# Optimization experiments

Hardware: AMD Instinct MI355X
Metric: run time of the kernel (lower is better)

The kernel has to match this reference:

```python
import jax, jax.numpy as jnp
import numpy as np

N = 50000      # nodes
E = 800000     # edges per relation
R = 3          # relations
FEAT = 64      # feat_len
HID = 64       # h_dim
NUM_PRED = 5
S = 8192       # seeds


def setup_inputs() -> dict:
    key = jax.random.key(0)
    ks = jax.random.split(key, 24)
    p = lambda k, s: jax.random.normal(k, s, jnp.float32) * 0.05
    x = jax.random.normal(ks[0], (N, FEAT), jnp.float32)
    noise = jax.random.normal(ks[1], (N, HID), jnp.float32)
    seeds = jax.random.randint(ks[2], (S,), 0, N)
    edges = [jax.random.randint(ks[3 + i], (E,), 0, N) for i in range(2 * R)]
    return dict(
        x=x, noise=noise, seeds=seeds,
        src0=edges[0], dst0=edges[1], src1=edges[2], dst1=edges[3],
        src2=edges[4], dst2=edges[5],
        W_conv1=p(ks[9], (R, FEAT, HID)), b_conv1=jnp.zeros((HID,), jnp.float32),
        W_conv2=p(ks[10], (R, HID, HID)), b_conv2=jnp.zeros((HID,), jnp.float32),
        W_lin=p(ks[11], (HID, HID)), b_lin=jnp.zeros((HID,), jnp.float32),
        dW1=p(ks[12], (R, HID, 256)), db1=jnp.zeros((R, 256), jnp.float32),
        dW2=p(ks[13], (R, 256, 32)), db2=jnp.zeros((R, 32), jnp.float32),
        dW3=p(ks[14], (R, 32, 1)), db3=jnp.zeros((R, 1), jnp.float32),
        fW1=p(ks[15], (R, HID, 256)), fb1=jnp.zeros((R, 256), jnp.float32),
        fW2=p(ks[16], (R, 256, 2048)), fb2=jnp.zeros((R, 2048), jnp.float32),
        fW3=p(ks[17], (R, 2048, FEAT * NUM_PRED)), fb3=jnp.zeros((R, FEAT * NUM_PRED), jnp.float32),
    )


def _rel_conv(h, srcs, dsts, W, b):
    # DGL RelGraphConvLayer: per-relation GraphConv(norm='right'), summed over
    # relations (HeteroGraphConv aggregate='sum'), + bias, ReLU (dropout=0).
    out_dim = W.shape[2]
    acc = jnp.zeros((N, out_dim), h.dtype)
    for r in range(R):
        m = (h @ W[r])[srcs[r]]                                   # [E, out]
        agg = jnp.zeros((N, out_dim), h.dtype).at[dsts[r]].add(m)
        deg = jnp.zeros((N,), h.dtype).at[dsts[r]].add(1.0)
        acc = acc + agg / jnp.maximum(deg, 1.0)[:, None]          # norm='right'
    return jax.nn.relu(acc + b)


def reference(x, noise, W_conv1, b_conv1, W_conv2, b_conv2, W_lin, b_lin,
              dW1, db1, dW2, db2, dW3, db3,
              fW1, fb1, fW2, fb2, fW3, fb3,
              seeds, src0, dst0, src1, dst1, src2, dst2):
    srcs = (src0, src1, src2)
    dsts = (dst0, dst1, dst2)
    # two stacked relational conv layers
    h = _rel_conv(x, srcs, dsts, W_conv1, b_conv1)
    h = _rel_conv(h, srcs, dsts, W_conv2, b_conv2)
    # per-ntype Linear + LeakyReLU (dropout=0)
    h = jax.nn.leaky_relu(h @ W_lin + b_lin)
    # Sampler: additive Gaussian noise
    h = h + noise
    # dGen/fGen index inputs[ntype][ind] with ind = enumerate position -> first S rows
    hs = h[:seeds.shape[0]]                                       # [S, HID]
    # ReldGen: per-relation MLP HID->256->32->1 (LeakyReLU, final ReLU)
    z = jax.nn.leaky_relu(jnp.einsum('sd,rdh->rsh', hs, dW1) + db1[:, None, :])
    z = jax.nn.leaky_relu(jnp.einsum('rsh,rhk->rsk', z, dW2) + db2[:, None, :])
    pred_missing = jax.nn.relu(jnp.einsum('rsk,rko->rso', z, dW3) + db3[:, None, :])  # [R,S,1]
    # RelfGen: per-relation MLP HID->256->2048->FEAT*NUM_PRED (ReLU, final Tanh)
    z = jax.nn.relu(jnp.einsum('sd,rdh->rsh', hs, fW1) + fb1[:, None, :])
    z = jax.nn.relu(jnp.einsum('rsh,rhk->rsk', z, fW2) + fb2[:, None, :])
    pred_feat = jnp.tanh(jnp.einsum('rsk,rko->rso', z, fW3) + fb3[:, None, :])        # [R,S,NUM_PRED*FEAT]
    # pack (pred_missing, pred_feat) into one array [R, S, 1 + NUM_PRED*FEAT]
    return jnp.concatenate([pred_missing, pred_feat], axis=-1)
```

## Files before the change

### kernel.cpp

```cpp
#include <hip/hip_runtime.h>
#include <math.h>

#define N_NODES 50000
#define N_EDGES 800000
#define RELS    3
#define HID     64
#define S_SEEDS 8192
#define OUT_COLS 321
#define S_CH    4096
#define NB      391
#define BCAP    2560
#define CHUNK   4096
#define NCHUNK  196

typedef __attribute__((ext_vector_type(8))) _Float16 v8h;
typedef __attribute__((ext_vector_type(4))) float v4f;

__device__ __forceinline__ unsigned short f32_to_f16(float f) {
    _Float16 h = (_Float16)f;
    return __builtin_bit_cast(unsigned short, h);
}
__device__ __forceinline__ float f16_to_f32(unsigned short u) {
    return (float)__builtin_bit_cast(_Float16, u);
}

template<int ACT, bool OUT_F16, int BN, int BM = 128>
__global__ __launch_bounds__(256) void gemm_mfma_f16(
    const unsigned short* __restrict__ A, long long sAb, int lda,
    const unsigned short* __restrict__ Bt, long long sBb,
    const float* __restrict__ bias, long long sBiasb,
    void* __restrict__ Cv, long long sCb, int ldc,
    const float* __restrict__ noise,
    int M, int Nc, int K)
{
    constexpr int WC = (BN == 128 || BM == 64) ? 2 : 1;
    constexpr int WR = 4 / WC;
    constexpr int TI = BM / (WR * 16);
    constexpr int TJ = BN / (WC * 16);
    constexpr int TPRA = 256 / BM;
    constexpr int TPRB = 256 / BN;

    __shared__ __align__(16) unsigned short As[2][BM][40];
    __shared__ __align__(16) unsigned short Bs[2][BN][40];

    const int r = blockIdx.z;
    A  += (long long)r * sAb;
    Bt += (long long)r * sBb;
    const float* brow = bias ? bias + (long long)r * sBiasb : nullptr;

    const int tid  = threadIdx.x;
    const int wave = tid >> 6, lane = tid & 63;
    const int quad = lane >> 4, l16 = lane & 15;
    const int wrow = (wave / WC) * (TI * 16);
    const int wcol = (wave % WC) * (TJ * 16);
    const int row0 = blockIdx.y * BM, col0 = blockIdx.x * BN;

    v4f acc[TI][TJ] = {};

    const int srow = tid / TPRA;
    const int ecol = (tid % TPRA) * (32 / TPRA);
    const int brw  = tid / TPRB;
    const int bcl  = (tid % TPRB) * (32 / TPRB);

    const int gr = row0 + srow;
    const bool aval = (gr < M);
    const unsigned short* aptr = A + (long long)gr * lda + ecol;
    const int gn = col0 + brw;
    const bool bval = (gn < Nc);
    const unsigned short* bptr = Bt + (long long)gn * K + bcl;

    int4 a0, a1, b0, b1;
    auto loadT = [&](int k0) {
        a0 = make_int4(0, 0, 0, 0); a1 = make_int4(0, 0, 0, 0);
        b0 = make_int4(0, 0, 0, 0); b1 = make_int4(0, 0, 0, 0);
        if (aval) {
            a0 = *(const int4*)(aptr + k0);
            if constexpr (TPRA == 2) a1 = *(const int4*)(aptr + k0 + 8);
        }
        if (bval) {
            b0 = *(const int4*)(bptr + k0);
            if constexpr (TPRB == 2) b1 = *(const int4*)(bptr + k0 + 8);
        }
    };
    auto storeT = [&](int buf) {
        *(int4*)(&As[buf][srow][ecol]) = a0;
        if constexpr (TPRA == 2) *(int4*)(&As[buf][srow][ecol + 8]) = a1;
        *(int4*)(&Bs[buf][brw][bcl]) = b0;
        if constexpr (TPRB == 2) *(int4*)(&Bs[buf][brw][bcl + 8]) = b1;
    };
    auto compute = [&](int buf) {
        v8h af[TI], bfr[TJ];
#pragma unroll
        for (int i = 0; i < TI; i++)
            af[i] = *(const v8h*)(&As[buf][wrow + i * 16 + l16][quad * 8]);
#pragma unroll
        for (int j = 0; j < TJ; j++)
            bfr[j] = *(const v8h*)(&Bs[buf][wcol + j * 16 + l16][quad * 8]);
#pragma unroll
        for (int i = 0; i < TI; i++)
#pragma unroll
            for (int j = 0; j < TJ; j++)
                acc[i][j] = __builtin_amdgcn_mfma_f32_16x16x32_f16(af[i], bfr[j], acc[i][j], 0, 0, 0);
    };

    loadT(0);
    storeT(0);
    __syncthreads();

    int cur = 0;
    for (int k0 = 32; k0 < K; k0 += 32) {
        loadT(k0);
        compute(cur);
        storeT(cur ^ 1);
        __syncthreads();
        cur ^= 1;
    }
    compute(cur);

    float* Cf = (float*)Cv + (long long)r * sCb;
    unsigned short* Ch = (unsigned short*)Cv + (long long)r * sCb;
#pragma unroll
    for (int i = 0; i < TI; i++) {
#pragma unroll
        for (int j = 0; j < TJ; j++) {
            int gc = col0 + wcol + j * 16 + l16;
            if (gc >= Nc) continue;
            float bv = brow ? brow[gc] : 0.f;
#pragma unroll
            for (int t = 0; t < 4; t++) {
                int grr = row0 + wrow + i * 16 + quad * 4 + t;
                if (grr >= M) continue;
                float v = acc[i][j][t] + bv;
                if (ACT == 1)      v = fmaxf(v, 0.f);
                else if (ACT == 2) v = (v > 0.f) ? v : 0.01f * v;
                else if (ACT == 3) v = tanhf(v);
                if (noise) v += noise[(long long)grr * ldc + gc];
                if (OUT_F16) Ch[(long long)grr * ldc + gc] = f32_to_f16(v);
                else         Cf[(long long)grr * ldc + gc] = v;
            }
        }
    }
}

__global__ void cvt_f32_f16_kernel(const float* __restrict__ src,
                                   unsigned short* __restrict__ dst, long long n)
{
    long long i = (long long)blockIdx.x * blockDim.x + threadIdx.x;
    if (i < n) dst[i] = f32_to_f16(src[i]);
}

struct TD { const float* s; unsigned short* d; int K, N, nbx, nby, b0; };
struct TDs { TD v[8]; };

__global__ __launch_bounds__(256) void transpose_all_kernel(TDs ds)
{
    __shared__ float t[32][33];
    int b = blockIdx.x;
    int k = 0;
#pragma unroll
    for (int q = 1; q < 8; q++) if (b >= ds.v[q].b0) k = q;
    TD td = ds.v[k];
    int local = b - td.b0;
    int per_r = td.nbx * td.nby;
    int r  = local / per_r;
    int rem = local - r * per_r;
    int by = rem / td.nbx, bx = rem - by * td.nbx;

    const float* src = td.s + (long long)r * td.K * td.N;
    unsigned short* dst = td.d + (long long)r * td.K * td.N;
    int n0 = bx * 32, k0 = by * 32;
    int tx = threadIdx.x & 31, ty = threadIdx.x >> 5;
#pragma unroll
    for (int i = 0; i < 32; i += 8) {
        int kk = k0 + ty + i, n = n0 + tx;
        if (kk < td.K && n < td.N) t[ty + i][tx] = src[(long long)kk * td.N + n];
    }
    __syncthreads();
#pragma unroll
    for (int i = 0; i < 32; i += 8) {
        int n = n0 + ty + i, kk = k0 + tx;
        if (n < td.N && kk < td.K) dst[(long long)n * td.K + kk] = f32_to_f16(t[tx][ty + i]);
    }
}

__global__ __launch_bounds__(256) void bin_fill_kernel(
    const int* __restrict__ s0, const int* __restrict__ d0,
    const int* __restrict__ s1, const int* __restrict__ d1,
    const int* __restrict__ s2, const int* __restrict__ d2,
    int* __restrict__ gcursor,
    unsigned int* __restrict__ bedges)
{
    __shared__ int cnt[NB];
    __shared__ int lstart[NB];
    __shared__ int fillc[NB];
    __shared__ int gstart[NB];
    __shared__ int scan[512];
    __shared__ unsigned int svals[CHUNK];
    __shared__ short sbuck[CHUNK];

    const int rel = blockIdx.y;
    const int* sp = (rel == 0) ? s0 : (rel == 1) ? s1 : s2;
    const int* dp = (rel == 0) ? d0 : (rel == 1) ? d1 : d2;
    const int tid = threadIdx.x;
    const int e0 = blockIdx.x * CHUNK;
    const int n  = min(CHUNK, N_EDGES - e0);

    for (int i = tid; i < NB; i += 256) { cnt[i] = 0; fillc[i] = 0; }
    __syncthreads();

    int myb[CHUNK / 256];
    unsigned int myv[CHUNK / 256];
#pragma unroll
    for (int i = 0; i < CHUNK / 256; i++) {
        int off = tid + i * 256;
        if (off < n) {
            int e = e0 + off;
            int s = sp[e], d = dp[e];
            int b = d >> 7;
            myb[i] = b;
            myv[i] = ((unsigned int)(d & 127) << 16) | (unsigned int)s;
            atomicAdd(&cnt[b], 1);
        } else myb[i] = -1;
    }
    __syncthreads();

    scan[tid]       = (tid < NB) ? cnt[tid] : 0;
    scan[tid + 256] = (tid + 256 < NB) ? cnt[tid + 256] : 0;
    __syncthreads();
    for (int off = 1; off < 512; off <<= 1) {
        int a = (tid >= off) ? scan[tid - off] : 0;
        int b = (tid + 256 >= off) ? scan[tid + 256 - off] : 0;
        __syncthreads();
        scan[tid] += a; scan[tid + 256] += b;
        __syncthreads();
    }
    if (tid < NB)       lstart[tid]       = scan[tid] - cnt[tid];
    if (tid + 256 < NB) lstart[tid + 256] = scan[tid + 256] - cnt[tid + 256];
    __syncthreads();

#pragma unroll
    for (int i = 0; i < CHUNK / 256; i++) {
        int b = myb[i];
        if (b >= 0) {
            int p = lstart[b] + atomicAdd(&fillc[b], 1);
            svals[p] = myv[i];
            sbuck[p] = (short)b;
        }
    }
    if (tid < NB && cnt[tid] > 0)
        gstart[tid] = atomicAdd(&gcursor[rel * NB + tid], cnt[tid]);
    if (tid + 256 < NB && cnt[tid + 256] > 0)
        gstart[tid + 256] = atomicAdd(&gcursor[rel * NB + tid + 256], cnt[tid + 256]);
    __syncthreads();

    for (int p = tid; p < n; p += 256) {
        int b = sbuck[p];
        int pos = gstart[b] + (p - lstart[b]);
        bedges[(long long)(rel * NB + b) * BCAP + pos] = svals[p];
    }
}

__global__ __launch_bounds__(256) void bucket_csr_kernel(
    const unsigned int* __restrict__ bedges,
    const int* __restrict__ gcursor,
    unsigned short* __restrict__ csr16,
    int* __restrict__ browptr)
{
    __shared__ int cnt[128], sc[128], start[128], cur[128];
    __shared__ unsigned short ssorted[BCAP];

    const int id  = blockIdx.y * NB + blockIdx.x;
    const int tid = threadIdx.x;
    const int len = gcursor[id];
    const unsigned int* ep = bedges + (long long)id * BCAP;

    for (int i = tid; i < 128; i += 256) cnt[i] = 0;
    __syncthreads();
    for (int i = tid; i < len; i += 256)
        atomicAdd(&cnt[ep[i] >> 16], 1);
    __syncthreads();

    int v = (tid < 128) ? cnt[tid] : 0;
    if (tid < 128) sc[tid] = v;
    __syncthreads();
    for (int off = 1; off < 128; off <<= 1) {
        int a = (tid < 128 && tid >= off) ? sc[tid - off] : 0;
        __syncthreads();
        if (tid < 128) sc[tid] += a;
        __syncthreads();
    }
    if (tid < 128) { start[tid] = sc[tid] - v; cur[tid] = sc[tid] - v; }
    __syncthreads();

    for (int i = tid; i < len; i += 256) {
        unsigned int vv = ep[i];
        int dl = vv >> 16;
        int pos = atomicAdd(&cur[dl], 1);
        ssorted[pos] = (unsigned short)(vv & 0xFFFFu);
    }
    __syncthreads();

    for (int i = tid; i < len; i += 256)
        csr16[(long long)id * BCAP + i] = ssorted[i];
    if (tid < 128) browptr[id * 128 + tid] = start[tid];
}

__global__ __launch_bounds__(256) void gather_csr_f16_kernel(
    const unsigned short* __restrict__ feat,
    const unsigned short* __restrict__ csr16,
    const int* __restrict__ browptr,
    const int* __restrict__ gcursor,
    unsigned short* __restrict__ agg,
    int M)
{
    int w = (blockIdx.x * 256 + threadIdx.x) >> 6;
    int lane = threadIdx.x & 63;
    if (w >= M * RELS) return;
    int r = w % RELS, d = w / RELS;
    int bucket = d >> 7, dl = d & 127;
    int id = r * NB + bucket;
    int p0 = browptr[id * 128 + dl];
    int p1 = (dl == 127) ? gcursor[id] : browptr[id * 128 + dl + 1];
    const unsigned short* cp = csr16 + (long long)id * BCAP;

    const int g   = lane >> 4;
    const unsigned fo = (unsigned)((lane & 15) << 2);

    float a0 = 0.f, a1 = 0.f, a2 = 0.f, a3 = 0.f;
    float b0 = 0.f, b1 = 0.f, b2 = 0.f, b3 = 0.f;
    int i = p0 + g;
    for (; i + 12 < p1; i += 16) {
        unsigned s0 = cp[i], s1 = cp[i + 4], s2 = cp[i + 8], s3 = cp[i + 12];
        ushort4 v0 = *(const ushort4*)(feat + (s0 << 6) + fo);
        ushort4 v1 = *(const ushort4*)(feat + (s1 << 6) + fo);
        ushort4 v2 = *(const ushort4*)(feat + (s2 << 6) + fo);
        ushort4 v3 = *(const ushort4*)(feat + (s3 << 6) + fo);
        a0 += f16_to_f32(v0.x) + f16_to_f32(v1.x);
        a1 += f16_to_f32(v0.y) + f16_to_f32(v1.y);
        a2 += f16_to_f32(v0.z) + f16_to_f32(v1.z);
        a3 += f16_to_f32(v0.w) + f16_to_f32(v1.w);
        b0 += f16_to_f32(v2.x) + f16_to_f32(v3.x);
        b1 += f16_to_f32(v2.y) + f16_to_f32(v3.y);
        b2 += f16_to_f32(v2.z) + f16_to_f32(v3.z);
        b3 += f16_to_f32(v2.w) + f16_to_f32(v3.w);
    }
    if (i + 4 < p1) {
        unsigned s0 = cp[i], s1 = cp[i + 4];
        ushort4 v0 = *(const ushort4*)(feat + (s0 << 6) + fo);
        ushort4 v1 = *(const ushort4*)(feat + (s1 << 6) + fo);
        a0 += f16_to_f32(v0.x) + f16_to_f32(v1.x);
        a1 += f16_to_f32(v0.y) + f16_to_f32(v1.y);
        a2 += f16_to_f32(v0.z) + f16_to_f32(v1.z);
        a3 += f16_to_f32(v0.w) + f16_to_f32(v1.w);
        i += 8;
    }
    if (i < p1) {
        unsigned s0 = cp[i];
        ushort4 v0 = *(const ushort4*)(feat + (s0 << 6) + fo);
        b0 += f16_to_f32(v0.x);
        b1 += f16_to_f32(v0.y);
        b2 += f16_to_f32(v0.z);
        b3 += f16_to_f32(v0.w);
    }
    a0 += b0; a1 += b1; a2 += b2; a3 += b3;

    a0 += __shfl_xor(a0, 16); a1 += __shfl_xor(a1, 16);
    a2 += __shfl_xor(a2, 16); a3 += __shfl_xor(a3, 16);
    a0 += __shfl_xor(a0, 32); a1 += __shfl_xor(a1, 32);
    a2 += __shfl_xor(a2, 32); a3 += __shfl_xor(a3, 32);

    if (lane < 16) {
        float inv = 1.0f / fmaxf((float)(p1 - p0), 1.0f);
        ushort4 o;
        o.x = f32_to_f16(a0 * inv);
        o.y = f32_to_f16(a1 * inv);
        o.z = f32_to_f16(a2 * inv);
        o.w = f32_to_f16(a3 * inv);
        *(ushort4*)(agg + (long long)d * (RELS * HID) + r * HID + fo) = o;
    }
}

__global__ void dhead_kernel(const float* __restrict__ z2d,
                             const float* __restrict__ dW3,
                             const float* __restrict__ db3,
                             float* __restrict__ out)
{
    int idx = blockIdx.x * blockDim.x + threadIdx.x;
    if (idx >= RELS * S_SEEDS) return;
    int r = idx / S_SEEDS;
    const float* zp = z2d + (long long)idx * 32;
    const float* wp = dW3 + r * 32;
    float acc = db3[r];
#pragma unroll
    for (int k = 0; k < 32; k++) acc += zp[k] * wp[k];
    out[(long long)idx * OUT_COLS] = fmaxf(acc, 0.f);
}

extern "C" void kernel_launch(void* const* d_in, const int* in_sizes, int n_in,
                              void* d_out, int out_size, void* d_ws, size_t ws_size,
                              hipStream_t stream)
{
    const float* x     = (const float*)d_in[0];
    const float* noise = (const float*)d_in[1];
    const int* srcs[RELS] = { (const int*)d_in[3], (const int*)d_in[5], (const int*)d_in[7] };
    const int* dsts[RELS] = { (const int*)d_in[4], (const int*)d_in[6], (const int*)d_in[8] };
    const float* Wc1  = (const float*)d_in[9];
    const float* bc1  = (const float*)d_in[10];
    const float* Wc2  = (const float*)d_in[11];
    const float* bc2  = (const float*)d_in[12];
    const float* Wlin = (const float*)d_in[13];
    const float* blin = (const float*)d_in[14];
    const float* dW1  = (const float*)d_in[15];
    const float* db1  = (const float*)d_in[16];
    const float* dW2  = (const float*)d_in[17];
    const float* db2  = (const float*)d_in[18];
    const float* dW3  = (const float*)d_in[19];
    const float* db3  = (const float*)d_in[20];
    const float* fW1  = (const float*)d_in[21];
    const float* fb1  = (const float*)d_in[22];
    const float* fW2  = (const float*)d_in[23];
    const float* fb2  = (const float*)d_in[24];
    const float* fW3  = (const float*)d_in[25];
    const float* fb3  = (const float*)d_in[26];
    float* out = (float*)d_out;
    float* w   = (float*)d_ws;

    int* gcursor = (int*)w;
    int* browptr = (int*)(w + 1280);
    unsigned short* csr16 = (unsigned short*)(w + 151424);
    unsigned short* aggx_hf = (unsigned short*)(w + 1652864);
    unsigned int*   bedges  = (unsigned int*)(w + 1652864 + 2400000);
    float*          z2d     = w + 1652864 + 2400000;
    unsigned short* z2hf    = (unsigned short*)(w + 1652864);
    unsigned short* xhf  = (unsigned short*)(w + 14235776);
    unsigned short* z1hf = (unsigned short*)(w + 14235776);
    unsigned short* h1hf   = (unsigned short*)(w + 17381504);
    unsigned short* agg2hf = (unsigned short*)(w + 18981504);
    unsigned short* h2shf  = (unsigned short*)(w + 19767936);
    unsigned short* hshf   = (unsigned short*)(w + 20030080);
    unsigned short* WcT1   = (unsigned short*)(w + 20292224);
    unsigned short* WcT2   = (unsigned short*)(w + 20298368);
    unsigned short* WlinT  = (unsigned short*)(w + 20304512);
    unsigned short* dW1ht  = (unsigned short*)(w + 20306560);
    unsigned short* dW2ht  = (unsigned short*)(w + 20331136);
    unsigned short* fW1ht  = (unsigned short*)(w + 20343424);
    unsigned short* fW2ht  = (unsigned short*)(w + 20368000);
    unsigned short* fW3ht  = (unsigned short*)(w + 21154432);

    hipMemsetAsync(gcursor, 0, (size_t)RELS * NB * sizeof(int), stream);
    bin_fill_kernel<<<dim3(NCHUNK, RELS), 256, 0, stream>>>(
        srcs[0], dsts[0], srcs[1], dsts[1], srcs[2], dsts[2], gcursor, bedges);
    bucket_csr_kernel<<<dim3(NB, RELS), 256, 0, stream>>>(
        bedges, gcursor, csr16, browptr);

    cvt_f32_f16_kernel<<<(N_NODES * HID + 255) / 256, 256, 0, stream>>>(x, xhf, (long long)N_NODES * HID);
    {
        TDs ds;
        int b0 = 0;
        auto add = [&](int k, const float* s, unsigned short* d, int K, int N, int rels) {
            ds.v[k].s = s; ds.v[k].d = d; ds.v[k].K = K; ds.v[k].N = N;
            ds.v[k].nbx = (N + 31) / 32; ds.v[k].nby = (K + 31) / 32; ds.v[k].b0 = b0;
            b0 += ds.v[k].nbx * ds.v[k].nby * rels;
        };
        add(0, Wc1, WcT1, 192, 64, 1);
        add(1, Wc2, WcT2, 192, 64, 1);
        add(2, Wlin, WlinT, 64, 64, 1);
        add(3, dW1, dW1ht, 64, 256, RELS);
        add(4, dW2, dW2ht, 256, 32, RELS);
        add(5, fW1, fW1ht, 64, 256, RELS);
        add(6, fW2, fW2ht, 256, 2048, RELS);
        add(7, fW3, fW3ht, 2048, 320, RELS);
        transpose_all_kernel<<<b0, 256, 0, stream>>>(ds);
    }

    gather_csr_f16_kernel<<<(N_NODES * RELS * 64 + 255) / 256, 256, 0, stream>>>(
        xhf, csr16, browptr, gcursor, aggx_hf, N_NODES);
    gemm_mfma_f16<1, true, 64, 64><<<dim3(1, (N_NODES + 63) / 64, 1), 256, 0, stream>>>(
        aggx_hf, 0, RELS * HID, WcT1, 0, bc1, 0,
        h1hf, 0, HID, nullptr, N_NODES, HID, RELS * HID);

    gather_csr_f16_kernel<<<(S_SEEDS * RELS * 64 + 255) / 256, 256, 0, stream>>>(
        h1hf, csr16, browptr, gcursor, agg2hf, S_SEEDS);
    gemm_mfma_f16<1, true, 64, 64><<<dim3(1, S_SEEDS / 64, 1), 256, 0, stream>>>(
        agg2hf, 0, RELS * HID, WcT2, 0, bc2, 0,
        h2shf, 0, HID, nullptr, S_SEEDS, HID, RELS * HID);

    gemm_mfma_f16<2, true, 64, 64><<<dim3(1, S_SEEDS / 64, 1), 256, 0, stream>>>(
        h2shf, 0, HID, WlinT, 0, blin, 0,
        hshf, 0, HID, noise, S_SEEDS, HID, HID);

    gemm_mfma_f16<2, true, 128><<<dim3(2, S_SEEDS / 128, RELS), 256, 0, stream>>>(
        hshf, 0, HID, dW1ht, 256LL * 64, db1, 256,
        z1hf, (long long)S_SEEDS * 256, 256, nullptr, S_SEEDS, 256, HID);
    gemm_mfma_f16<2, false, 64, 64><<<dim3(1, S_SEEDS / 64, RELS), 256, 0, stream>>>(
        z1hf, (long long)S_SEEDS * 256, 256, dW2ht, 32LL * 256, db2, 32,
        z2d, (long long)S_SEEDS * 32, 32, nullptr, S_SEEDS, 32, 256);
    dhead_kernel<<<(RELS * S_SEEDS + 255) / 256, 256, 0, stream>>>(z2d, dW3, db3, out);

    gemm_mfma_f16<1, true, 128><<<dim3(2, S_SEEDS / 128, RELS), 256, 0, stream>>>(
        hshf, 0, HID, fW1ht, 256LL * 64, fb1, 256,
        z1hf, (long long)S_SEEDS * 256, 256, nullptr, S_SEEDS, 256, HID);
    for (int c = 0; c < S_SEEDS / S_CH; c++) {
        long long s0 = (long long)c * S_CH;
        gemm_mfma_f16<1, true, 128><<<dim3(2048 / 128, S_CH / 128, RELS), 256, 0, stream>>>(
            z1hf + s0 * 256, (long long)S_SEEDS * 256, 256,
            fW2ht, 2048LL * 256, fb2, 2048,
            z2hf, (long long)S_CH * 2048, 2048, nullptr, S_CH, 2048, 256);
        gemm_mfma_f16<3, false, 64, 64><<<dim3(5, S_CH / 64, RELS), 256, 0, stream>>>(
            z2hf, (long long)S_CH * 2048, 2048,
            fW3ht, 320LL * 2048, fb3, 320,
            out + s0 * OUT_COLS + 1, (long long)S_SEEDS * OUT_COLS, OUT_COLS,
            nullptr, S_CH, 320, 2048);
    }
}
```

Measured before the change: 512.7 us.

## Remap GEMM blocks across XCDs and gather all relations per wave in packed fp16

The GEMM kernel now remaps block indices so consecutive tiles land on the same XCD chiplet, aiming for better L2 locality on the 8-XCD part. The CSR gather kernel now gives each wave one destination node and loops over all three relations, which cuts the wave count by three. It also accumulates neighbour features with packed half2 adds instead of fp32 scalar adds, reducing conversion and ALU work. In exchange, accumulating in fp16 loses precision and risks overflow on high-degree nodes, and each wave now handles more serial work.

```diff
diff --git a/kernel.cpp b/kernel.cpp
--- a/kernel.cpp
+++ b/kernel.cpp
@@ -15,6 +15,7 @@
 
 typedef __attribute__((ext_vector_type(8))) _Float16 v8h;
 typedef __attribute__((ext_vector_type(4))) float v4f;
+typedef __attribute__((ext_vector_type(2))) _Float16 h2;
 
 __device__ __forceinline__ unsigned short f32_to_f16(float f) {
     _Float16 h = (_Float16)f;
@@ -23,6 +24,8 @@
 __device__ __forceinline__ float f16_to_f32(unsigned short u) {
     return (float)__builtin_bit_cast(_Float16, u);
 }
+__device__ __forceinline__ h2 u2h2(unsigned u) { return __builtin_bit_cast(h2, u); }
+__device__ __forceinline__ unsigned h2u(h2 h) { return __builtin_bit_cast(unsigned, h); }
 
 template<int ACT, bool OUT_F16, int BN, int BM = 128>
 __global__ __launch_bounds__(256) void gemm_mfma_f16(
@@ -48,12 +51,23 @@
     Bt += (long long)r * sBb;
     const float* brow = bias ? bias + (long long)r * sBiasb : nullptr;
 
+    int bx = blockIdx.x, by = blockIdx.y;
+    {
+        const int nwg  = gridDim.x * gridDim.y;
+        const int orig = by * gridDim.x + bx;
+        const int q = nwg >> 3, rm = nwg & 7;
+        const int xcd = orig & 7, idx = orig >> 3;
+        const int wg = (xcd < rm ? xcd * (q + 1) : rm * (q + 1) + (xcd - rm) * q) + idx;
+        bx = wg % gridDim.x;
+        by = wg / gridDim.x;
+    }
+
     const int tid  = threadIdx.x;
     const int wave = tid >> 6, lane = tid & 63;
     const int quad = lane >> 4, l16 = lane & 15;
     const int wrow = (wave / WC) * (TI * 16);
     const int wcol = (wave % WC) * (TJ * 16);
-    const int row0 = blockIdx.y * BM, col0 = blockIdx.x * BN;
+    const int row0 = by * BM, col0 = bx * BN;
 
     v4f acc[TI][TJ] = {};
 
@@ -313,70 +327,70 @@
     unsigned short* __restrict__ agg,
     int M)
 {
-    int w = (blockIdx.x * 256 + threadIdx.x) >> 6;
+    int d = (blockIdx.x * 256 + threadIdx.x) >> 6;
     int lane = threadIdx.x & 63;
-    if (w >= M * RELS) return;
-    int r = w % RELS, d = w / RELS;
+    if (d >= M) return;
     int bucket = d >> 7, dl = d & 127;
-    int id = r * NB + bucket;
-    int p0 = browptr[id * 128 + dl];
-    int p1 = (dl == 127) ? gcursor[id] : browptr[id * 128 + dl + 1];
-    const unsigned short* cp = csr16 + (long long)id * BCAP;
-
-    const int g   = lane >> 4;
+    const int g = lane >> 4;
     const unsigned fo = (unsigned)((lane & 15) << 2);
 
-    float a0 = 0.f, a1 = 0.f, a2 = 0.f, a3 = 0.f;
-    float b0 = 0.f, b1 = 0.f, b2 = 0.f, b3 = 0.f;
-    int i = p0 + g;
-    for (; i + 12 < p1; i += 16) {
-        unsigned s0 = cp[i], s1 = cp[i + 4], s2 = cp[i + 8], s3 = cp[i + 12];
-        ushort4 v0 = *(const ushort4*)(feat + (s0 << 6) + fo);
-        ushort4 v1 = *(const ushort4*)(feat + (s1 << 6) + fo);
-        ushort4 v2 = *(const ushort4*)(feat + (s2 << 6) + fo);
-        ushort4 v3 = *(const ushort4*)(feat + (s3 << 6) + fo);
-        a0 += f16_to_f32(v0.x) + f16_to_f32(v1.x);
-        a1 += f16_to_f32(v0.y) + f16_to_f32(v1.y);
-        a2 += f16_to_f32(v0.z) + f16_to_f32(v1.z);
-        a3 += f16_to_f32(v0.w) + f16_to_f32(v1.w);
-        b0 += f16_to_f32(v2.x) + f16_to_f32(v3.x);
-        b1 += f16_to_f32(v2.y) + f16_to_f32(v3.y);
-        b2 += f16_to_f32(v2.z) + f16_to_f32(v3.z);
-        b3 += f16_to_f32(v2.w) + f16_to_f32(v3.w);
-    }
-    if (i + 4 < p1) {
-        unsigned s0 = cp[i], s1 = cp[i + 4];
-        ushort4 v0 = *(const ushort4*)(feat + (s0 << 6) + fo);
-        ushort4 v1 = *(const ushort4*)(feat + (s1 << 6) + fo);
-        a0 += f16_to_f32(v0.x) + f16_to_f32(v1.x);
-        a1 += f16_to_f32(v0.y) + f16_to_f32(v1.y);
-        a2 += f16_to_f32(v0.z) + f16_to_f32(v1.z);
-        a3 += f16_to_f32(v0.w) + f16_to_f32(v1.w);
-        i += 8;
-    }
-    if (i < p1) {
-        unsigned s0 = cp[i];
-        ushort4 v0 = *(const ushort4*)(feat + (s0 << 6) + fo);
-        b0 += f16_to_f32(v0.x);
-        b1 += f16_to_f32(v0.y);
-        b2 += f16_to_f32(v0.z);
-        b3 += f16_to_f32(v0.w);
-    }
-    a0 += b0; a1 += b1; a2 += b2; a3 += b3;
-
-    a0 += __shfl_xor(a0, 16); a1 += __shfl_xor(a1, 16);
-    a2 += __shfl_xor(a2, 16); a3 += __shfl_xor(a3, 16);
-    a0 += __shfl_xor(a0, 32); a1 += __shfl_xor(a1, 32);
-    a2 += __shfl_xor(a2, 32); a3 += __shfl_xor(a3, 32);
-
-    if (lane < 16) {
-        float inv = 1.0f / fmaxf((float)(p1 - p0), 1.0f);
-        ushort4 o;
-        o.x = f32_to_f16(a0 * inv);
-        o.y = f32_to_f16(a1 * inv);
-        o.z = f32_to_f16(a2 * inv);
-        o.w = f32_to_f16(a3 * inv);
-        *(ushort4*)(agg + (long long)d * (RELS * HID) + r * HID + fo) = o;
+    int p0[RELS], p1[RELS];
+#pragma unroll
+    for (int r = 0; r < RELS; r++) {
+        int id = r * NB + bucket;
+        p0[r] = browptr[id * 128 + dl];
+        p1[r] = (dl == 127) ? gcursor[id] : browptr[id * 128 + dl + 1];
+    }
+
+    unsigned short* outp = agg + (long long)d * (RELS * HID);
+
+#pragma unroll
+    for (int r = 0; r < RELS; r++) {
+        const unsigned short* cp = csr16 + (long long)(r * NB + bucket) * BCAP;
+        h2 aA01 = (h2)0, aA23 = (h2)0, aB01 = (h2)0, aB23 = (h2)0;
+        const int e1 = p1[r];
+        int i = p0[r] + g;
+        for (; i + 12 < e1; i += 16) {
+            unsigned s0 = cp[i], s1 = cp[i + 4], s2 = cp[i + 8], s3 = cp[i + 12];
+            uint2 w0 = *(const uint2*)(feat + (s0 << 6) + fo);
+            uint2 w1 = *(const uint2*)(feat + (s1 << 6) + fo);
+            uint2 w2 = *(const uint2*)(feat + (s2 << 6) + fo);
+            uint2 w3 = *(const uint2*)(feat + (s3 << 6) + fo);
+            aA01 += u2h2(w0.x) + u2h2(w1.x);
+            aA23 += u2h2(w0.y) + u2h2(w1.y);
+            aB01 += u2h2(w2.x) + u2h2(w3.x);
+            aB23 += u2h2(w2.y) + u2h2(w3.y);
+        }
+        if (i + 4 < e1) {
+            unsigned s0 = cp[i], s1 = cp[i + 4];
+            uint2 w0 = *(const uint2*)(feat + (s0 << 6) + fo);
+            uint2 w1 = *(const uint2*)(feat + (s1 << 6) + fo);
+            aA01 += u2h2(w0.x) + u2h2(w1.x);
+            aA23 += u2h2(w0.y) + u2h2(w1.y);
+            i += 8;
+        }
+        if (i < e1) {
+            unsigned s0 = cp[i];
+            uint2 w0 = *(const uint2*)(feat + (s0 << 6) + fo);
+            aB01 += u2h2(w0.x);
+            aB23 += u2h2(w0.y);
+        }
+        h2 a01 = aA01 + aB01, a23 = aA23 + aB23;
+
+        a01 += u2h2((unsigned)__shfl_xor((int)h2u(a01), 16));
+        a23 += u2h2((unsigned)__shfl_xor((int)h2u(a23), 16));
+        a01 += u2h2((unsigned)__shfl_xor((int)h2u(a01), 32));
+        a23 += u2h2((unsigned)__shfl_xor((int)h2u(a23), 32));
+
+        if (lane < 16) {
+            float inv = 1.0f / fmaxf((float)(e1 - p0[r]), 1.0f);
+            ushort4 o;
+            o.x = f32_to_f16((float)a01.x * inv);
+            o.y = f32_to_f16((float)a01.y * inv);
+            o.z = f32_to_f16((float)a23.x * inv);
+            o.w = f32_to_f16((float)a23.y * inv);
+            *(ushort4*)(outp + r * HID + fo) = o;
+        }
     }
 }
 
@@ -473,13 +487,13 @@
         transpose_all_kernel<<<b0, 256, 0, stream>>>(ds);
     }
 
-    gather_csr_f16_kernel<<<(N_NODES * RELS * 64 + 255) / 256, 256, 0, stream>>>(
+    gather_csr_f16_kernel<<<(N_NODES + 3) / 4, 256, 0, stream>>>(
         xhf, csr16, browptr, gcursor, aggx_hf, N_NODES);
     gemm_mfma_f16<1, true, 64, 64><<<dim3(1, (N_NODES + 63) / 64, 1), 256, 0, stream>>>(
         aggx_hf, 0, RELS * HID, WcT1, 0, bc1, 0,
         h1hf, 0, HID, nullptr, N_NODES, HID, RELS * HID);
 
-    gather_csr_f16_kernel<<<(S_SEEDS * RELS * 64 + 255) / 256, 256, 0, stream>>>(
+    gather_csr_f16_kernel<<<(S_SEEDS + 3) / 4, 256, 0, stream>>>(
         h1hf, csr16, browptr, gcursor, agg2hf, S_SEEDS);
     gemm_mfma_f16<1, true, 64, 64><<<dim3(1, S_SEEDS / 64, 1), 256, 0, stream>>>(
         agg2hf, 0, RELS * HID, WcT2, 0, bc2, 0,
```

After: 489.5 us. -4.5%, faster.
